# Performance work log

Measured on AMD Instinct MI355X. Metric: run time of the kernel, lower is better.

## Reference

```python
import jax, jax.numpy as jnp
import numpy as np

# Static per-expert capacities (tokens are laid out contiguously per expert)
CAPS = [1024, 512, 1024, 256, 1024, 512, 128, 1024, 512, 1024, 256, 512, 1024, 128, 64, 512]
TOTAL = sum(CAPS)  # 9536
E, H, I = 16, 1024, 4096
OFFSETS = np.concatenate([[0], np.cumsum(CAPS)])


def setup_inputs() -> dict:
    key = jax.random.key(0)
    ks = jax.random.split(key, 5)
    x = jax.random.normal(ks[0], (TOTAL, H), dtype=jnp.float32)
    W1 = jax.random.normal(ks[1], (E, I, H), dtype=jnp.float32) * 0.02
    b1 = jax.random.normal(ks[2], (E, I), dtype=jnp.float32) * 0.02
    W2 = jax.random.normal(ks[3], (E, H, I), dtype=jnp.float32) * 0.02
    b2 = jax.random.normal(ks[4], (E, H), dtype=jnp.float32) * 0.02
    return {"x": x, "W1": W1, "b1": b1, "W2": W2, "b2": b2}


def reference(x, W1, b1, W2, b2):
    # Grouped GEMM FFN: expert e processes rows [OFFSETS[e]:OFFSETS[e+1]]
    # out = gelu(x_e @ W1[e].T + b1[e]) @ W2[e].T + b2[e]
    outs = []
    for e in range(E):  # fixed, static loop over experts (capacities are static)
        xs = x[OFFSETS[e]:OFFSETS[e + 1]]                      # [cap_e, H]
        h = jax.nn.gelu(xs @ W1[e].T + b1[e], approximate=False)  # [cap_e, I]
        outs.append(h @ W2[e].T + b2[e])                       # [cap_e, H]
    return jnp.concatenate(outs, axis=0)                       # [TOTAL, H]
```

## Files before the change

kernel.cpp:

```cpp
#include <hip/hip_runtime.h>
#include <math.h>

typedef __attribute__((ext_vector_type(8))) short short8;
typedef __attribute__((ext_vector_type(4))) float f32x4;
typedef __attribute__((ext_vector_type(2))) unsigned int u32x2;
typedef __attribute__((ext_vector_type(4))) unsigned int u32x4;

#define E_NUM 16
constexpr int CAPS[E_NUM] = {1024,512,1024,256,1024,512,128,1024,512,1024,256,512,1024,128,64,512};
constexpr int OFFS[E_NUM] = {0,1024,1536,2560,2816,3840,4352,4480,5504,6016,7040,7296,7808,8832,8960,9024};
constexpr int cdiv_(int a, int b){ return (a + b - 1) / b; }
constexpr int ilog2_(int v){ int l = 0; while ((1 << l) < v) ++l; return l; }

__device__ __forceinline__ unsigned int cvt_pk_bf16(float a, float b){
  unsigned int r;
  asm("v_cvt_pk_bf16_f32 %0, %1, %2" : "=v"(r) : "v"(a), "v"(b));
  return r;
}

typedef __attribute__((address_space(1))) const unsigned char gas_u8;
typedef __attribute__((address_space(3))) unsigned char las_u8;
__device__ __forceinline__ void gl_lds16(const void* g, void* l){
  __builtin_amdgcn_global_load_lds((gas_u8*)g, (las_u8*)l, 16, 0, 0);
}

__global__ __launch_bounds__(256) void cvt_bf16_kernel(const float* __restrict__ x,
                                                       unsigned short* __restrict__ xb, int n8)
{
  int i = blockIdx.x * blockDim.x + threadIdx.x;
  const int stride = gridDim.x * blockDim.x;
  for (; i < n8; i += stride) {
    f32x4 a = *reinterpret_cast<const f32x4*>(x + (size_t)i * 8);
    f32x4 b = *reinterpret_cast<const f32x4*>(x + (size_t)i * 8 + 4);
    u32x2 lo, hi;
    lo[0] = cvt_pk_bf16(a[0], a[1]); lo[1] = cvt_pk_bf16(a[2], a[3]);
    hi[0] = cvt_pk_bf16(b[0], b[1]); hi[1] = cvt_pk_bf16(b[2], b[3]);
    *reinterpret_cast<u32x2*>(xb + (size_t)i * 8)     = lo;
    *reinterpret_cast<u32x2*>(xb + (size_t)i * 8 + 4) = hi;
  }
}

template<bool A_GLDS, bool GELU_OUT, int TM, int NDIM, int KDIM, int LOG_GN, int NWG, int KS>
__global__ __launch_bounds__(256, 3)
void expert_gemm(const void* __restrict__ Av, const float* __restrict__ W,
                 const float* __restrict__ bias, void* __restrict__ Outv)
{
  constexpr int A_BYTES = TM * 64;
  constexpr int B_BYTES = 128 * 128;
  constexpr int GN   = 1 << LOG_GN;
  constexpr int MFR  = TM / 32;
  constexpr int NT   = KDIM / (KS * 32);
  constexpr int NWG1 = NWG / KS;
  static_assert(NWG % 8 == 0, "grid must be divisible by 8 for XCD swizzle");
  static_assert(!GELU_OUT || (2 * A_BYTES + 2 * B_BYTES) >= 128 * 128 * 2, "GELU needs 32KB");
  static_assert(!GELU_OUT || KS == 1, "GELU path is KS=1 only");

  __shared__ __align__(16) char smem[2 * A_BYTES + 2 * B_BYTES];

  const int tid  = threadIdx.x;
  const int braw = blockIdx.x;
  const int t = (braw & 7) * (NWG / 8) + (braw >> 3);

  const int kc    = t / NWG1;
  const int tt    = t % NWG1;
  const int kbase = kc * (KDIM / KS);

  int m0 = 0, n0 = 0, Me = 0, tok0 = 0;
  size_t wbase = 0, bbase = 0;
  {
    int acc0 = 0;
    #pragma unroll
    for (int i = 0; i < E_NUM; ++i) {
      const int mt  = cdiv_(CAPS[i], TM);
      const int lmt = ilog2_(mt);
      const int nb  = mt * (NDIM / 128);
      if (tt >= acc0 && tt < acc0 + nb) {
        const int loc = tt - acc0;
        const int g   = loc >> (lmt + LOG_GN);
        const int rem = loc & ((mt << LOG_GN) - 1);
        m0   = (rem >> LOG_GN) * TM;
        n0   = ((g << LOG_GN) | (rem & (GN - 1))) * 128;
        Me   = CAPS[i];
        tok0 = OFFS[i];
        wbase = (size_t)i * NDIM * KDIM;
        bbase = (size_t)i * NDIM;
      }
      acc0 += nb;
    }
  }
  const float* Wb = W + wbase;

  const int lane = tid & 63;
  const int wv   = tid >> 6;

  const unsigned short* Ah = (const unsigned short*)Av;
  const float*          Af = (const float*)Av;

  auto stageB = [&](int buf, int kt) {
    const float* Bg = Wb + (size_t)n0 * KDIM + kbase + kt * 32;
    char* dst0 = smem + 2 * A_BYTES + buf * B_BYTES;
    #pragma unroll
    for (int j = 0; j < 4; ++j) {
      const int rbase = wv * 32 + j * 8;
      const int r     = rbase + (lane >> 3);
      const int lblk  = (lane & 7) ^ (r & 7);
      gl_lds16((const void*)(Bg + (size_t)r * KDIM + lblk * 4), (void*)(dst0 + rbase * 128));
    }
  };

  auto stageA = [&](int buf, int kt) {
    const unsigned short* Ag = Ah + (size_t)(tok0 + m0) * KDIM + kbase + kt * 32;
    char* dst0 = smem + buf * A_BYTES;
    #pragma unroll
    for (int j = 0; j < TM / 64; ++j) {
      const int rbase = wv * (TM / 4) + j * 16;
      const int r     = rbase + (lane >> 2);
      const int lblk  = (lane & 3) ^ (r & 3);
      gl_lds16((const void*)(Ag + (size_t)r * KDIM + lblk * 8), (void*)(dst0 + rbase * 64));
    }
  };

  const int sr = tid >> 3;
  const int sc = (tid & 7) * 8;
  f32x4 ra[MFR];
  auto loadA_reg = [&](int kt) {
    const int k0 = kbase + kt * 32;
    #pragma unroll
    for (int i = 0; i < MFR; ++i)
      ra[i] = *reinterpret_cast<const f32x4*>(Af + (size_t)(tok0 + m0 + sr + 32 * i) * KDIM + k0 + (sc >> 1));
  };
  auto writeA_reg = [&](int buf) {
    char* ab = smem + buf * A_BYTES;
    #pragma unroll
    for (int i = 0; i < MFR; ++i) {
      u32x2 p;
      p[0] = cvt_pk_bf16(ra[i][0], ra[i][1]);
      p[1] = cvt_pk_bf16(ra[i][2], ra[i][3]);
      *reinterpret_cast<u32x2*>(ab + (sr + 32 * i) * 64 + (sc ^ ((sr & 3) << 4))) = p;
    }
  };

  const int wm   = (wv >> 1) * (TM / 2);
  const int wn   = (wv & 1) * 64;
  const int lrow = lane & 15;
  const int pa0  = (((lane >> 4) ^ (lane & 3)) << 4);
  const int pb0  = ((((lane >> 4) << 1) ^ (lane & 7)) << 4);

  f32x4 acc_[MFR][4];
  #pragma unroll
  for (int i = 0; i < MFR; ++i)
    #pragma unroll
    for (int j = 0; j < 4; ++j)
      acc_[i][j] = (f32x4){0.f, 0.f, 0.f, 0.f};

  auto mfma_step = [&](int cur) {
    const char* ab  = smem + cur * A_BYTES;
    const char* bbp = smem + 2 * A_BYTES + cur * B_BYTES;
    short8 afr[MFR], bfr[4];
    #pragma unroll
    for (int f = 0; f < MFR; ++f)
      afr[f] = *reinterpret_cast<const short8*>(ab + (wm + f * 16 + lrow) * 64 + pa0);
    #pragma unroll
    for (int f = 0; f < 4; ++f) {
      const char* rowp = bbp + (size_t)(wn + f * 16 + lrow) * 128;
      f32x4 lo = *reinterpret_cast<const f32x4*>(rowp + pb0);
      f32x4 hi = *reinterpret_cast<const f32x4*>(rowp + (pb0 ^ 16));
      u32x4 pk;
      pk[0] = cvt_pk_bf16(lo[0], lo[1]);
      pk[1] = cvt_pk_bf16(lo[2], lo[3]);
      pk[2] = cvt_pk_bf16(hi[0], hi[1]);
      pk[3] = cvt_pk_bf16(hi[2], hi[3]);
      bfr[f] = __builtin_bit_cast(short8, pk);
    }
    #pragma unroll
    for (int i = 0; i < MFR; ++i)
      #pragma unroll
      for (int j = 0; j < 4; ++j)
        acc_[i][j] = __builtin_amdgcn_mfma_f32_16x16x32_bf16(afr[i], bfr[j], acc_[i][j], 0, 0, 0);
  };

  if constexpr (A_GLDS) stageA(0, 0); else { loadA_reg(0); writeA_reg(0); }
  stageB(0, 0);
  __syncthreads();

  for (int kt = 0; kt < NT; ++kt) {
    const int cur = kt & 1;
    if (kt + 1 < NT) {
      stageB(cur ^ 1, kt + 1);
      if constexpr (A_GLDS) stageA(cur ^ 1, kt + 1);
      else                  loadA_reg(kt + 1);
    }
    mfma_step(cur);
    if constexpr (!A_GLDS) { if (kt + 1 < NT) writeA_reg(cur ^ 1); }
    __syncthreads();
  }

  float bv[4];
  #pragma unroll
  for (int f = 0; f < 4; ++f)
    bv[f] = bias[bbase + n0 + wn + f * 16 + lrow];

  if constexpr (GELU_OUT) {
    static_assert(TM == 128, "GELU path assumes 128-row tiles");
    unsigned short* hout = (unsigned short*)smem;
    #pragma unroll
    for (int i = 0; i < MFR; ++i) {
      const int rbase = wm + i * 16 + (lane >> 4) * 4;
      #pragma unroll
      for (int j = 0; j < 4; ++j) {
        #pragma unroll
        for (int jj = 0; jj < 4; ++jj) {
          float xv = acc_[i][j][jj] + bv[j];
          float y2 = xv * (1.5957691216057308f + 0.07135481627f * xv * xv);
          float g  = xv * __builtin_amdgcn_rcpf(1.0f + __expf(-y2));
          hout[(rbase + jj) * 128 + wn + j * 16 + lrow] = (unsigned short)(cvt_pk_bf16(g, g) & 0xFFFFu);
        }
      }
    }
    __syncthreads();
    unsigned short* Oh = (unsigned short*)Outv;
    #pragma unroll
    for (int it = 0; it < 8; ++it) {
      int row  = it * 16 + (tid >> 4);
      int c    = (tid & 15) * 8;
      int grow = m0 + row;
      if (grow < Me) {
        *reinterpret_cast<short8*>(Oh + (size_t)(tok0 + grow) * NDIM + n0 + c)
          = *reinterpret_cast<const short8*>(hout + row * 128 + c);
      }
    }
  } else {
    float* Of = (float*)Outv;
    constexpr float BS = 1.0f / (float)KS;
    #pragma unroll
    for (int i = 0; i < MFR; ++i) {
      const int rbase = wm + i * 16 + (lane >> 4) * 4;
      #pragma unroll
      for (int jj = 0; jj < 4; ++jj) {
        int grow = m0 + rbase + jj;
        if (grow < Me) {
          #pragma unroll
          for (int j = 0; j < 4; ++j) {
            float v = acc_[i][j][jj] + bv[j] * BS;
            float* p = Of + (size_t)(tok0 + grow) * NDIM + n0 + wn + j * 16 + lrow;
            if constexpr (KS > 1) unsafeAtomicAdd(p, v);
            else                  *p = v;
          }
        }
      }
    }
  }
}

extern "C" void kernel_launch(void* const* d_in, const int* in_sizes, int n_in,
                              void* d_out, int out_size, void* d_ws, size_t ws_size,
                              hipStream_t stream)
{
  const float* x  = (const float*)d_in[0];
  const float* W1 = (const float*)d_in[1];
  const float* b1 = (const float*)d_in[2];
  const float* W2 = (const float*)d_in[3];
  const float* b2 = (const float*)d_in[4];
  float* out = (float*)d_out;

  constexpr size_t H_BYTES  = (size_t)9536 * 4096 * 2;
  constexpr size_t XB_BYTES = (size_t)9536 * 1024 * 2;
  unsigned short* h  = (unsigned short*)d_ws;
  unsigned short* xb = (unsigned short*)((char*)d_ws + H_BYTES);

  const bool use_xb = ws_size >= H_BYTES + XB_BYTES;

  hipMemsetAsync(d_out, 0, (size_t)out_size * sizeof(float), stream);

  if (use_xb) {
    cvt_bf16_kernel<<<2048, 256, 0, stream>>>(x, xb, 9536 * 1024 / 8);
    expert_gemm<true, true, 128, 4096, 1024, 2, 75 * 32, 1>
        <<<75 * 32, 256, 0, stream>>>((const void*)xb, W1, b1, (void*)h);
  } else {
    expert_gemm<false, true, 128, 4096, 1024, 2, 75 * 32, 1>
        <<<75 * 32, 256, 0, stream>>>((const void*)x, W1, b1, (void*)h);
  }

  expert_gemm<true, false, 128, 1024, 4096, 0, 2 * 75 * 8, 2>
      <<<2 * 75 * 8, 256, 0, stream>>>((const void*)h, W2, b2, (void*)out);
}
```

Measured before the change: 371.6 us.

## Use 256x256 tiles with 512-thread blocks and triple-buffered LDS pipeline

Replaces the 128x128 expert GEMM kernel with a 256x256-tile variant using 8 waves per block. The bf16-A path gets a three-stage LDS pipeline with explicit vmcnt waits and barriers. The second GEMM switches from 2-way to 4-way K-split with atomics. Larger tiles cut how often W and A are re-read from global memory, but they raise register and LDS pressure and make expert tails with small capacities pad up to 256 rows, wasting work.

```diff
diff --git a/kernel.cpp b/kernel.cpp
--- a/kernel.cpp
+++ b/kernel.cpp
@@ -40,22 +40,22 @@
   }
 }
 
-template<bool A_GLDS, bool GELU_OUT, int TM, int NDIM, int KDIM, int LOG_GN, int NWG, int KS>
-__global__ __launch_bounds__(256, 3)
-void expert_gemm(const void* __restrict__ Av, const float* __restrict__ W,
-                 const float* __restrict__ bias, void* __restrict__ Outv)
+template<bool A_BF16, bool GELU_OUT, int NDIM, int KDIM, int LOG_GN, int NWG, int KS>
+__global__ __launch_bounds__(512, 2)
+void expert_gemm256(const void* __restrict__ Av, const float* __restrict__ W,
+                    const float* __restrict__ bias, void* __restrict__ Outv)
 {
-  constexpr int A_BYTES = TM * 64;
-  constexpr int B_BYTES = 128 * 128;
+  constexpr int A_BYTES = 256 * 64;
+  constexpr int B_BYTES = 256 * 128;
+  constexpr int BUF  = A_BYTES + B_BYTES;
+  constexpr int NBUF = A_BF16 ? 3 : 2;
   constexpr int GN   = 1 << LOG_GN;
-  constexpr int MFR  = TM / 32;
-  constexpr int NT   = KDIM / (KS * 32);
+  constexpr int NTT  = KDIM / (KS * 32);
   constexpr int NWG1 = NWG / KS;
   static_assert(NWG % 8 == 0, "grid must be divisible by 8 for XCD swizzle");
-  static_assert(!GELU_OUT || (2 * A_BYTES + 2 * B_BYTES) >= 128 * 128 * 2, "GELU needs 32KB");
-  static_assert(!GELU_OUT || KS == 1, "GELU path is KS=1 only");
-
-  __shared__ __align__(16) char smem[2 * A_BYTES + 2 * B_BYTES];
+  static_assert(NTT >= 3, "pipeline needs >=3 K-steps");
+
+  __shared__ __align__(16) char smem[NBUF * BUF];
 
   const int tid  = threadIdx.x;
   const int braw = blockIdx.x;
@@ -71,15 +71,15 @@
     int acc0 = 0;
     #pragma unroll
     for (int i = 0; i < E_NUM; ++i) {
-      const int mt  = cdiv_(CAPS[i], TM);
+      const int mt  = cdiv_(CAPS[i], 256);
       const int lmt = ilog2_(mt);
-      const int nb  = mt * (NDIM / 128);
+      const int nb  = mt * (NDIM / 256);
       if (tt >= acc0 && tt < acc0 + nb) {
         const int loc = tt - acc0;
         const int g   = loc >> (lmt + LOG_GN);
         const int rem = loc & ((mt << LOG_GN) - 1);
-        m0   = (rem >> LOG_GN) * TM;
-        n0   = ((g << LOG_GN) | (rem & (GN - 1))) * 128;
+        m0   = (rem >> LOG_GN) * 256;
+        n0   = ((g << LOG_GN) | (rem & (GN - 1))) * 256;
         Me   = CAPS[i];
         tok0 = OFFS[i];
         wbase = (size_t)i * NDIM * KDIM;
@@ -96,103 +96,112 @@
   const unsigned short* Ah = (const unsigned short*)Av;
   const float*          Af = (const float*)Av;
 
+  auto stageA = [&](int buf, int kt) {
+    const unsigned short* Ag = Ah + (size_t)(tok0 + m0) * KDIM + kbase + kt * 32;
+    char* dst0 = smem + buf * BUF;
+    #pragma unroll
+    for (int j = 0; j < 2; ++j) {
+      const int rbase = j * 128 + wv * 16;
+      const int r     = rbase + (lane >> 2);
+      const int blk   = (lane & 3) ^ (r & 3);
+      gl_lds16((const void*)(Ag + (size_t)r * KDIM + blk * 8), (void*)(dst0 + rbase * 64));
+    }
+  };
   auto stageB = [&](int buf, int kt) {
     const float* Bg = Wb + (size_t)n0 * KDIM + kbase + kt * 32;
-    char* dst0 = smem + 2 * A_BYTES + buf * B_BYTES;
+    char* dst0 = smem + buf * BUF + A_BYTES;
     #pragma unroll
     for (int j = 0; j < 4; ++j) {
-      const int rbase = wv * 32 + j * 8;
+      const int rbase = j * 64 + wv * 8;
       const int r     = rbase + (lane >> 3);
-      const int lblk  = (lane & 7) ^ (r & 7);
-      gl_lds16((const void*)(Bg + (size_t)r * KDIM + lblk * 4), (void*)(dst0 + rbase * 128));
-    }
-  };
-
-  auto stageA = [&](int buf, int kt) {
-    const unsigned short* Ag = Ah + (size_t)(tok0 + m0) * KDIM + kbase + kt * 32;
-    char* dst0 = smem + buf * A_BYTES;
-    #pragma unroll
-    for (int j = 0; j < TM / 64; ++j) {
-      const int rbase = wv * (TM / 4) + j * 16;
-      const int r     = rbase + (lane >> 2);
-      const int lblk  = (lane & 3) ^ (r & 3);
-      gl_lds16((const void*)(Ag + (size_t)r * KDIM + lblk * 8), (void*)(dst0 + rbase * 64));
-    }
-  };
-
-  const int sr = tid >> 3;
-  const int sc = (tid & 7) * 8;
-  f32x4 ra[MFR];
+      const int blk   = (lane & 7) ^ (r & 7);
+      gl_lds16((const void*)(Bg + (size_t)r * KDIM + blk * 4), (void*)(dst0 + rbase * 128));
+    }
+  };
+
+  const int fr = tid >> 1;
+  const int fcq = (tid & 1) * 2;
+  f32x4 raf[4];
   auto loadA_reg = [&](int kt) {
-    const int k0 = kbase + kt * 32;
-    #pragma unroll
-    for (int i = 0; i < MFR; ++i)
-      ra[i] = *reinterpret_cast<const f32x4*>(Af + (size_t)(tok0 + m0 + sr + 32 * i) * KDIM + k0 + (sc >> 1));
+    const float* Ap = Af + (size_t)(tok0 + m0 + fr) * KDIM + kbase + kt * 32 + fcq * 8;
+    #pragma unroll
+    for (int i = 0; i < 4; ++i)
+      raf[i] = *reinterpret_cast<const f32x4*>(Ap + i * 4);
   };
   auto writeA_reg = [&](int buf) {
-    char* ab = smem + buf * A_BYTES;
-    #pragma unroll
-    for (int i = 0; i < MFR; ++i) {
+    char* ab = smem + buf * BUF;
+    #pragma unroll
+    for (int i = 0; i < 2; ++i) {
       u32x2 p;
-      p[0] = cvt_pk_bf16(ra[i][0], ra[i][1]);
-      p[1] = cvt_pk_bf16(ra[i][2], ra[i][3]);
-      *reinterpret_cast<u32x2*>(ab + (sr + 32 * i) * 64 + (sc ^ ((sr & 3) << 4))) = p;
-    }
-  };
-
-  const int wm   = (wv >> 1) * (TM / 2);
-  const int wn   = (wv & 1) * 64;
+      p[0] = cvt_pk_bf16(raf[2*i][0], raf[2*i][1]);
+      p[1] = cvt_pk_bf16(raf[2*i][2], raf[2*i][3]);
+      const int blk = (fcq + i) ^ (fr & 3);
+      *reinterpret_cast<u32x2*>(ab + fr * 64 + blk * 16) = p;
+    }
+  };
+
+  const int wm   = (wv >> 2) * 128;
+  const int wn   = (wv & 3) * 64;
   const int lrow = lane & 15;
   const int pa0  = (((lane >> 4) ^ (lane & 3)) << 4);
   const int pb0  = ((((lane >> 4) << 1) ^ (lane & 7)) << 4);
 
-  f32x4 acc_[MFR][4];
+  f32x4 acc_[8][4];
   #pragma unroll
-  for (int i = 0; i < MFR; ++i)
+  for (int i = 0; i < 8; ++i)
     #pragma unroll
     for (int j = 0; j < 4; ++j)
       acc_[i][j] = (f32x4){0.f, 0.f, 0.f, 0.f};
 
-  auto mfma_step = [&](int cur) {
-    const char* ab  = smem + cur * A_BYTES;
-    const char* bbp = smem + 2 * A_BYTES + cur * B_BYTES;
-    short8 afr[MFR], bfr[4];
-    #pragma unroll
-    for (int f = 0; f < MFR; ++f)
-      afr[f] = *reinterpret_cast<const short8*>(ab + (wm + f * 16 + lrow) * 64 + pa0);
+  auto compute = [&](int cur) {
+    const char* ab  = smem + cur * BUF;
+    const char* bbp = smem + cur * BUF + A_BYTES;
+    short8 bfr[4];
     #pragma unroll
     for (int f = 0; f < 4; ++f) {
       const char* rowp = bbp + (size_t)(wn + f * 16 + lrow) * 128;
       f32x4 lo = *reinterpret_cast<const f32x4*>(rowp + pb0);
       f32x4 hi = *reinterpret_cast<const f32x4*>(rowp + (pb0 ^ 16));
       u32x4 pk;
-      pk[0] = cvt_pk_bf16(lo[0], lo[1]);
-      pk[1] = cvt_pk_bf16(lo[2], lo[3]);
-      pk[2] = cvt_pk_bf16(hi[0], hi[1]);
-      pk[3] = cvt_pk_bf16(hi[2], hi[3]);
+      pk[0] = cvt_pk_bf16(lo[0], lo[1]); pk[1] = cvt_pk_bf16(lo[2], lo[3]);
+      pk[2] = cvt_pk_bf16(hi[0], hi[1]); pk[3] = cvt_pk_bf16(hi[2], hi[3]);
       bfr[f] = __builtin_bit_cast(short8, pk);
     }
     #pragma unroll
-    for (int i = 0; i < MFR; ++i)
+    for (int i = 0; i < 8; ++i) {
+      short8 afr = *reinterpret_cast<const short8*>(ab + (wm + i * 16 + lrow) * 64 + pa0);
       #pragma unroll
       for (int j = 0; j < 4; ++j)
-        acc_[i][j] = __builtin_amdgcn_mfma_f32_16x16x32_bf16(afr[i], bfr[j], acc_[i][j], 0, 0, 0);
-  };
-
-  if constexpr (A_GLDS) stageA(0, 0); else { loadA_reg(0); writeA_reg(0); }
-  stageB(0, 0);
-  __syncthreads();
-
-  for (int kt = 0; kt < NT; ++kt) {
-    const int cur = kt & 1;
-    if (kt + 1 < NT) {
-      stageB(cur ^ 1, kt + 1);
-      if constexpr (A_GLDS) stageA(cur ^ 1, kt + 1);
-      else                  loadA_reg(kt + 1);
-    }
-    mfma_step(cur);
-    if constexpr (!A_GLDS) { if (kt + 1 < NT) writeA_reg(cur ^ 1); }
+        acc_[i][j] = __builtin_amdgcn_mfma_f32_16x16x32_bf16(afr, bfr[j], acc_[i][j], 0, 0, 0);
+    }
+  };
+
+  if constexpr (A_BF16) {
+    stageA(0, 0); stageB(0, 0);
+    stageA(1, 1); stageB(1, 1);
+    int cur = 0, nx2 = 2;
+    for (int kt = 0; kt < NTT; ++kt) {
+      if (kt + 1 < NTT) {
+        asm volatile("s_waitcnt vmcnt(6)\n\ts_barrier" ::: "memory");
+      } else {
+        asm volatile("s_waitcnt vmcnt(0)\n\ts_barrier" ::: "memory");
+      }
+      __builtin_amdgcn_sched_barrier(0);
+      if (kt + 2 < NTT) { stageA(nx2, kt + 2); stageB(nx2, kt + 2); }
+      compute(cur);
+      cur = (cur == 2) ? 0 : cur + 1;
+      nx2 = (nx2 == 2) ? 0 : nx2 + 1;
+    }
+  } else {
+    loadA_reg(0); stageB(0, 0); writeA_reg(0);
     __syncthreads();
+    for (int kt = 0; kt < NTT; ++kt) {
+      const int cur = kt & 1;
+      if (kt + 1 < NTT) { stageB(cur ^ 1, kt + 1); loadA_reg(kt + 1); }
+      compute(cur);
+      if (kt + 1 < NTT) writeA_reg(cur ^ 1);
+      __syncthreads();
+    }
   }
 
   float bv[4];
@@ -201,39 +210,59 @@
     bv[f] = bias[bbase + n0 + wn + f * 16 + lrow];
 
   if constexpr (GELU_OUT) {
-    static_assert(TM == 128, "GELU path assumes 128-row tiles");
-    unsigned short* hout = (unsigned short*)smem;
-    #pragma unroll
-    for (int i = 0; i < MFR; ++i) {
-      const int rbase = wm + i * 16 + (lane >> 4) * 4;
-      #pragma unroll
-      for (int j = 0; j < 4; ++j) {
+    unsigned short* Oh = (unsigned short*)Outv;
+    if constexpr (A_BF16) {
+      __syncthreads();
+      unsigned short* hout = (unsigned short*)smem;
+      #pragma unroll
+      for (int i = 0; i < 8; ++i) {
+        const int rbase = wm + i * 16 + (lane >> 4) * 4;
         #pragma unroll
-        for (int jj = 0; jj < 4; ++jj) {
-          float xv = acc_[i][j][jj] + bv[j];
-          float y2 = xv * (1.5957691216057308f + 0.07135481627f * xv * xv);
-          float g  = xv * __builtin_amdgcn_rcpf(1.0f + __expf(-y2));
-          hout[(rbase + jj) * 128 + wn + j * 16 + lrow] = (unsigned short)(cvt_pk_bf16(g, g) & 0xFFFFu);
+        for (int j = 0; j < 4; ++j) {
+          #pragma unroll
+          for (int jj = 0; jj < 4; ++jj) {
+            float xv = acc_[i][j][jj] + bv[j];
+            float y2 = xv * (1.5957691216057308f + 0.07135481627f * xv * xv);
+            float g  = xv * __builtin_amdgcn_rcpf(1.0f + __expf(-y2));
+            hout[(rbase + jj) * 256 + wn + j * 16 + lrow] = (unsigned short)(cvt_pk_bf16(g, g) & 0xFFFFu);
+          }
         }
       }
-    }
-    __syncthreads();
-    unsigned short* Oh = (unsigned short*)Outv;
-    #pragma unroll
-    for (int it = 0; it < 8; ++it) {
-      int row  = it * 16 + (tid >> 4);
-      int c    = (tid & 15) * 8;
-      int grow = m0 + row;
-      if (grow < Me) {
-        *reinterpret_cast<short8*>(Oh + (size_t)(tok0 + grow) * NDIM + n0 + c)
-          = *reinterpret_cast<const short8*>(hout + row * 128 + c);
+      __syncthreads();
+      #pragma unroll
+      for (int s = 0; s < 16; ++s) {
+        const int row = s * 16 + (tid >> 5);
+        const int c   = (tid & 31) * 8;
+        if (m0 + row < Me) {
+          *reinterpret_cast<short8*>(Oh + (size_t)(tok0 + m0 + row) * NDIM + n0 + c)
+            = *reinterpret_cast<const short8*>(hout + row * 256 + c);
+        }
+      }
+    } else {
+      #pragma unroll
+      for (int i = 0; i < 8; ++i) {
+        const int rbase = wm + i * 16 + (lane >> 4) * 4;
+        #pragma unroll
+        for (int j = 0; j < 4; ++j) {
+          #pragma unroll
+          for (int jj = 0; jj < 4; ++jj) {
+            int grow = m0 + rbase + jj;
+            if (grow < Me) {
+              float xv = acc_[i][j][jj] + bv[j];
+              float y2 = xv * (1.5957691216057308f + 0.07135481627f * xv * xv);
+              float g  = xv * __builtin_amdgcn_rcpf(1.0f + __expf(-y2));
+              Oh[(size_t)(tok0 + grow) * NDIM + n0 + wn + j * 16 + lrow]
+                = (unsigned short)(cvt_pk_bf16(g, g) & 0xFFFFu);
+            }
+          }
+        }
       }
     }
   } else {
     float* Of = (float*)Outv;
     constexpr float BS = 1.0f / (float)KS;
     #pragma unroll
-    for (int i = 0; i < MFR; ++i) {
+    for (int i = 0; i < 8; ++i) {
       const int rbase = wm + i * 16 + (lane >> 4) * 4;
       #pragma unroll
       for (int jj = 0; jj < 4; ++jj) {
@@ -274,13 +303,13 @@
 
   if (use_xb) {
     cvt_bf16_kernel<<<2048, 256, 0, stream>>>(x, xb, 9536 * 1024 / 8);
-    expert_gemm<true, true, 128, 4096, 1024, 2, 75 * 32, 1>
-        <<<75 * 32, 256, 0, stream>>>((const void*)xb, W1, b1, (void*)h);
+    expert_gemm256<true, true, 4096, 1024, 2, 624, 1>
+        <<<624, 512, 0, stream>>>((const void*)xb, W1, b1, (void*)h);
   } else {
-    expert_gemm<false, true, 128, 4096, 1024, 2, 75 * 32, 1>
-        <<<75 * 32, 256, 0, stream>>>((const void*)x, W1, b1, (void*)h);
-  }
-
-  expert_gemm<true, false, 128, 1024, 4096, 0, 2 * 75 * 8, 2>
-      <<<2 * 75 * 8, 256, 0, stream>>>((const void*)h, W2, b2, (void*)out);
-}
+    expert_gemm256<false, true, 4096, 1024, 2, 624, 1>
+        <<<624, 512, 0, stream>>>((const void*)x, W1, b1, (void*)h);
+  }
+
+  expert_gemm256<true, false, 1024, 4096, 2, 624, 4>
+      <<<624, 512, 0, stream>>>((const void*)h, W2, b2, (void*)out);
+}
```

Result: slower. 398.0 us (+7.1%).
